# Kernel optimization log

Hardware: AMD Instinct MI355X
Metric: run time of the kernel (lower is better)

## Reference

```python
import jax, jax.numpy as jnp
import numpy as np

NUM_QUERIES = 10000
NUM_CLASSES = 2048
IOU_THRESH = 0.5


def setup_inputs() -> dict:
    key = jax.random.key(0)
    k1, k2, k3, k4 = jax.random.split(key, 4)
    return {
        "pred_logits": jax.random.normal(k1, (1, NUM_QUERIES, NUM_CLASSES), dtype=jnp.float32),
        "pred_boxes": jax.random.uniform(k2, (1, NUM_QUERIES, 4), dtype=jnp.float32),
        "cls_logits": jax.random.normal(k3, (1, NUM_CLASSES), dtype=jnp.float32),
        "target_sizes": jax.random.randint(k4, (1, 2), 480, 1333, dtype=jnp.int64),
    }


def box_cxcywh_to_xyxy(b):
    cx, cy, w, h = b[..., 0], b[..., 1], b[..., 2], b[..., 3]
    return jnp.stack([cx - 0.5 * w, cy - 0.5 * h, cx + 0.5 * w, cy + 0.5 * h], axis=-1)


def nms_keep(boxes, scores, iou_thresh):
    """Greedy NMS; returns a boolean keep mask over the N boxes (xyxy)."""
    n = boxes.shape[0]
    order = jnp.argsort(-scores)
    bs = boxes[order]  # [N,4] sorted by score desc
    areas = jnp.clip(bs[:, 2] - bs[:, 0], 0.0) * jnp.clip(bs[:, 3] - bs[:, 1], 0.0)
    idx = jnp.arange(n)

    def body(i, state):
        keep_s, active = state
        alive = active[i]
        keep_s = keep_s.at[i].set(alive)
        # IoU of box i against all boxes
        lt = jnp.maximum(bs[i, :2], bs[:, :2])
        rb = jnp.minimum(bs[i, 2:], bs[:, 2:])
        wh = jnp.clip(rb - lt, 0.0)
        inter = wh[:, 0] * wh[:, 1]
        iou = inter / (areas[i] + areas - inter)
        suppress = (iou > iou_thresh) & (idx > i) & alive
        return keep_s, active & (~suppress)

    keep_s, _ = jax.lax.fori_loop(
        0, n, body, (jnp.zeros(n, dtype=bool), jnp.ones(n, dtype=bool))
    )
    # map back from sorted order to original order
    return jnp.zeros(n, dtype=bool).at[order].set(keep_s)


def reference(pred_logits, pred_boxes, cls_logits, target_sizes):
    # class scores / labels
    prob = jax.nn.softmax(pred_logits, axis=-1)          # [B,Q,C]
    scores = prob.max(axis=-1)                           # [B,Q]
    labels = prob.argmax(axis=-1)                        # [B,Q]
    cls_preds = jnp.argmax(cls_logits, axis=1)           # [B]

    # boxes: cxcywh -> xyxy, clamp to [0,1], scale to image size
    boxes = jnp.clip(box_cxcywh_to_xyxy(pred_boxes), 0.0, 1.0)  # [B,Q,4]
    ts = target_sizes.astype(jnp.float32)
    img_h, img_w = ts[:, 0], ts[:, 1]
    scale_fct = jnp.stack([img_w, img_h, img_w, img_h], axis=1)  # [B,4]
    boxes = boxes * scale_fct[:, None, :]

    # greedy NMS on batch 0 (module only supports this path for B=1)
    keep = nms_keep(boxes[0], scores.reshape(-1), IOU_THRESH)    # [Q] bool

    return scores[0], labels[0], boxes[0], keep, cls_preds
```

## Files before the change

kernel.cpp:

```cpp
#include <hip/hip_runtime.h>
#include <stdint.h>

#define NQ 10000
#define NC 2048
#define NW 157
#define NR 79
#define IOU_TH 0.5f


__global__ __launch_bounds__(256) void k_scores(const float* __restrict__ logits,
        float* __restrict__ out_scores, float* __restrict__ out_labels,
        float* __restrict__ ws_scores) {
    int wave = threadIdx.x >> 6;
    int lane = threadIdx.x & 63;
    int q = blockIdx.x * 4 + wave;
    if (q >= NQ) return;
    const float* row = logits + (size_t)q * NC;
    float4 v[8];
    float m = -3.4e38f;
    int am = 0;
    #pragma unroll
    for (int k = 0; k < 8; k++) {
        int idx = k * 256 + lane * 4;
        v[k] = *(const float4*)(row + idx);
        if (v[k].x > m) { m = v[k].x; am = idx; }
        if (v[k].y > m) { m = v[k].y; am = idx + 1; }
        if (v[k].z > m) { m = v[k].z; am = idx + 2; }
        if (v[k].w > m) { m = v[k].w; am = idx + 3; }
    }
    #pragma unroll
    for (int off = 32; off >= 1; off >>= 1) {
        float om = __shfl_xor(m, off);
        int   oa = __shfl_xor(am, off);
        if (om > m || (om == m && oa < am)) { m = om; am = oa; }
    }
    float s = 0.f;
    #pragma unroll
    for (int k = 0; k < 8; k++) {
        s += expf(v[k].x - m);
        s += expf(v[k].y - m);
        s += expf(v[k].z - m);
        s += expf(v[k].w - m);
    }
    #pragma unroll
    for (int off = 32; off >= 1; off >>= 1) s += __shfl_xor(s, off);
    if (lane == 0) {
        float sc = 1.0f / s;
        out_scores[q] = sc;
        out_labels[q] = (float)am;
        ws_scores[q]  = sc;
    }
}

__global__ __launch_bounds__(256) void k_cls(const float* __restrict__ cls,
                                             float* __restrict__ out) {
    float m = -3.4e38f; int am = 0x7fffffff;
    for (int idx = threadIdx.x; idx < NC; idx += 256) {
        float x = cls[idx];
        if (x > m) { m = x; am = idx; }
    }
    int lane = threadIdx.x & 63, wave = threadIdx.x >> 6;
    #pragma unroll
    for (int off = 32; off >= 1; off >>= 1) {
        float om = __shfl_xor(m, off); int oa = __shfl_xor(am, off);
        if (om > m || (om == m && oa < am)) { m = om; am = oa; }
    }
    __shared__ float sm[4]; __shared__ int sa[4];
    if (lane == 0) { sm[wave] = m; sa[wave] = am; }
    __syncthreads();
    if (threadIdx.x == 0) {
        for (int w = 1; w < 4; w++)
            if (sm[w] > m || (sm[w] == m && sa[w] < am)) { m = sm[w]; am = sa[w]; }
        out[0] = (float)am;
    }
}

__global__ __launch_bounds__(256) void k_boxes(const float* __restrict__ pb,
        const int* __restrict__ ts, float* __restrict__ out_boxes,
        float* __restrict__ boxes4, int* __restrict__ rank) {
    #pragma clang fp contract(off)
    int i = blockIdx.x * 256 + threadIdx.x;
    if (i >= NQ) return;
    rank[i] = 0;
    int a0 = ts[0], a1 = ts[1];
    int ih, iw;
    if (a1 == 0) { ih = a0; iw = ts[2]; } else { ih = a0; iw = a1; }
    float sh = (float)ih, sw = (float)iw;
    float4 b = *(const float4*)(pb + i * 4);
    float x1 = b.x - 0.5f * b.z;
    float y1 = b.y - 0.5f * b.w;
    float x2 = b.x + 0.5f * b.z;
    float y2 = b.y + 0.5f * b.w;
    x1 = fminf(fmaxf(x1, 0.f), 1.f) * sw;
    y1 = fminf(fmaxf(y1, 0.f), 1.f) * sh;
    x2 = fminf(fmaxf(x2, 0.f), 1.f) * sw;
    y2 = fminf(fmaxf(y2, 0.f), 1.f) * sh;
    float4 o = make_float4(x1, y1, x2, y2);
    *(float4*)(out_boxes + i * 4) = o;
    *(float4*)(boxes4 + i * 4) = o;
}

__global__ __launch_bounds__(256) void k_count(const float* __restrict__ scores,
                                               int* __restrict__ rank) {
    __shared__ float sc[2000];
    int jbase = blockIdx.y * 2000;
    int jn = min(2000, NQ - jbase);
    for (int t = threadIdx.x; t < jn; t += 256) sc[t] = scores[jbase + t];
    __syncthreads();
    int i = blockIdx.x * 256 + threadIdx.x;
    if (i >= NQ) return;
    float si = scores[i];
    int cnt = 0;
    for (int jj = 0; jj < jn; jj++) {
        float sj = sc[jj];
        int j = jbase + jj;
        cnt += (sj > si) || (sj == si && j < i);
    }
    if (cnt) atomicAdd(&rank[i], cnt);
}

__global__ __launch_bounds__(256) void k_scatter(const float* __restrict__ boxes4,
        const int* __restrict__ rank, int* __restrict__ order,
        float* __restrict__ sx1, float* __restrict__ sy1,
        float* __restrict__ sx2, float* __restrict__ sy2,
        float* __restrict__ sarea) {
    #pragma clang fp contract(off)
    int i = blockIdx.x * 256 + threadIdx.x;
    if (i >= NQ) return;
    int r = rank[i];
    order[r] = i;
    float4 b = *(const float4*)(boxes4 + i * 4);
    sx1[r] = b.x; sy1[r] = b.y; sx2[r] = b.z; sy2[r] = b.w;
    sarea[r] = fmaxf(b.z - b.x, 0.f) * fmaxf(b.w - b.y, 0.f);
}

__global__ __launch_bounds__(64) void k_mask(const float* __restrict__ sx1,
        const float* __restrict__ sy1, const float* __restrict__ sx2,
        const float* __restrict__ sy2, const float* __restrict__ sarea,
        unsigned long long* __restrict__ mask) {
    #pragma clang fp contract(off)
    int rb = blockIdx.x, cb = blockIdx.y;
    if (cb < rb) return;
    int t = threadIdx.x;
    __shared__ float cx1[64], cy1[64], cx2[64], cy2[64], ca[64];
    int j0 = cb * 64 + t;
    if (j0 < NQ) { cx1[t]=sx1[j0]; cy1[t]=sy1[j0]; cx2[t]=sx2[j0]; cy2[t]=sy2[j0]; ca[t]=sarea[j0]; }
    __syncthreads();
    int i = rb * 64 + t;
    if (i >= NQ) return;
    float xi1 = sx1[i], yi1 = sy1[i], xi2 = sx2[i], yi2 = sy2[i], ai = sarea[i];
    int ncol = min(64, NQ - cb * 64);
    unsigned long long word = 0;
    for (int jj = 0; jj < ncol; jj++) {
        int j = cb * 64 + jj;
        float lx = fmaxf(xi1, cx1[jj]);
        float ly = fmaxf(yi1, cy1[jj]);
        float rx = fminf(xi2, cx2[jj]);
        float ry = fminf(yi2, cy2[jj]);
        float w = fmaxf(rx - lx, 0.f);
        float h = fmaxf(ry - ly, 0.f);
        float inter = w * h;
        float denom = (ai + ca[jj]) - inter;
        float iou = inter / denom;
        bool sup = (iou > IOU_TH) && (j > i);
        word |= ((unsigned long long)(sup ? 1u : 0u)) << jj;
    }
    mask[(size_t)i * NW + cb] = word;
}

__device__ __forceinline__ unsigned long long bcast64(unsigned long long v) {
    uint32_t lo = (uint32_t)__builtin_amdgcn_readfirstlane((int)(uint32_t)v);
    uint32_t hi = (uint32_t)__builtin_amdgcn_readfirstlane((int)(uint32_t)(v >> 32));
    return ((unsigned long long)hi << 32) | lo;
}

__global__ __launch_bounds__(256, 1) void k_scan(const unsigned long long* __restrict__ mask,
        const int* __restrict__ order, float* __restrict__ out_keep) {
    __shared__ unsigned long long rem[NW];
    __shared__ unsigned long long keepw[NW];
    __shared__ unsigned long long stA[2][4][64];
    __shared__ unsigned long long stB[2][3][64];
    __shared__ unsigned long long sh_k0, sh_k1;

    const int tid  = threadIdx.x;
    const int wave = tid >> 6;
    const int lane = tid & 63;

    for (int w = tid; w < NW; w += 256) rem[w] = 0;

    if (wave == 1) {
        uint64_t sA0=0,sA1=0,sA2=0,sA3=0,sB0=0,sB1=0,sB2=0;
        int ra = lane, rb = 64 + lane;
        {
            const unsigned long long* rp = mask + (size_t)ra * NW;
            sA0 = rp[0]; sA1 = rp[1]; sA2 = rp[2]; sA3 = rp[3];
        }
        {
            const unsigned long long* rp = mask + (size_t)rb * NW;
            sB0 = rp[1]; sB1 = rp[2]; sB2 = rp[3];
        }
        stA[0][0][lane]=sA0; stA[0][1][lane]=sA1; stA[0][2][lane]=sA2; stA[0][3][lane]=sA3;
        stB[0][0][lane]=sB0; stB[0][1][lane]=sB1; stB[0][2][lane]=sB2;
    }
    __syncthreads();

    uint64_t pp0=0,pp1=0,pp2=0,pp3=0,pp4=0,pp5=0,pp6=0,pp7=0;
    uint64_t pp8=0,pp9=0,pp10=0,pp11=0,pp12=0,pp13=0,pp14=0,pp15=0;
    uint64_t pp16=0,pp17=0,pp18=0,pp19=0,pp20=0,pp21=0,pp22=0,pp23=0;
    uint64_t pp24=0,pp25=0,pp26=0,pp27=0,pp28=0,pp29=0,pp30=0,pp31=0;
    uint64_t pex = 0;
    int pw = -1;

    uint64_t kept0 = 0, kept1 = 0;

    for (int r = 0; r < NR; r++) {
        const int a = 2 * r, b = a + 1;
        const int par = r & 1;

        uint64_t sA0=0,sA1=0,sA2=0,sA3=0,sB0=0,sB1=0,sB2=0;

        if (wave == 0) {
            uint64_t remA_v = rem[a];
            uint64_t remB_v = (b < NW) ? rem[b] : ~0ull;
            uint64_t dgA = stA[par][0][lane];
            uint64_t xAB = stA[par][1][lane];
            uint64_t dgB = (b < NW) ? stB[par][0][lane] : 0;

            uint64_t cur0 = bcast64(remA_v);
            int nv0 = min(64, NQ - a * 64);
            if (nv0 < 64) cur0 |= (~0ull) << nv0;
            uint32_t dglo = (uint32_t)dgA, dghi = (uint32_t)(dgA >> 32);
            uint32_t xlo  = (uint32_t)xAB, xhi  = (uint32_t)(xAB >> 32);
            uint64_t alive = ~cur0;
            uint64_t k0 = 0, AcB = 0;
            while (alive) {
                int bb = (int)__builtin_ctzll(alive);
                uint64_t d = ((uint64_t)(uint32_t)__builtin_amdgcn_readlane((int)dghi, bb) << 32)
                           | (uint32_t)__builtin_amdgcn_readlane((int)dglo, bb);
                uint64_t x = ((uint64_t)(uint32_t)__builtin_amdgcn_readlane((int)xhi, bb) << 32)
                           | (uint32_t)__builtin_amdgcn_readlane((int)xlo, bb);
                k0    |= 1ull << bb;
                cur0  |= d;
                AcB   |= x;
                alive &= ~(d | (1ull << bb));
            }
            kept0 = k0;

            uint64_t k1 = 0, cur1 = 0;
            if (b < NW) {
                cur1 = bcast64(remB_v) | AcB;
                int nv1 = min(64, NQ - b * 64);
                if (nv1 < 64) cur1 |= (~0ull) << nv1;
                uint32_t blo = (uint32_t)dgB, bhi = (uint32_t)(dgB >> 32);
                uint64_t alv = ~cur1;
                while (alv) {
                    int bb = (int)__builtin_ctzll(alv);
                    uint64_t d = ((uint64_t)(uint32_t)__builtin_amdgcn_readlane((int)bhi, bb) << 32)
                               | (uint32_t)__builtin_amdgcn_readlane((int)blo, bb);
                    k1  |= 1ull << bb;
                    cur1 |= d;
                    alv &= ~(d | (1ull << bb));
                }
            }
            kept1 = k1;
            if (tid == 0) {
                sh_k0 = k0; sh_k1 = k1;
                keepw[a] = cur0;
                if (b < NW) keepw[b] = cur1;
            }
        } else {
            if (pw >= 0) {
                uint64_t pacc = (((pp0|pp1)|(pp2|pp3)) | ((pp4|pp5)|(pp6|pp7)))
                              | (((pp8|pp9)|(pp10|pp11)) | ((pp12|pp13)|(pp14|pp15)));
                pacc |= (((pp16|pp17)|(pp18|pp19)) | ((pp20|pp21)|(pp22|pp23)))
                      | (((pp24|pp25)|(pp26|pp27)) | ((pp28|pp29)|(pp30|pp31)));
                pacc |= pex;
                if (pacc) atomicOr(&rem[pw], (unsigned long long)pacc);
            }
            pw = -1;

            if (wave == 1) {
                int a2 = a + 2, b2 = a + 3;
                int ra = a2 * 64 + lane, rb = b2 * 64 + lane;
                if (a2 < NW && ra < NQ) {
                    const unsigned long long* rp = mask + (size_t)ra * NW + a2;
                    sA0 = rp[0];
                    if (a2 + 1 < NW) sA1 = rp[1];
                    if (a2 + 2 < NW) sA2 = rp[2];
                    if (a2 + 3 < NW) sA3 = rp[3];
                }
                if (b2 < NW && rb < NQ) {
                    const unsigned long long* rp = mask + (size_t)rb * NW + b2;
                    sB0 = rp[0];
                    if (b2 + 1 < NW) sB1 = rp[1];
                    if (b2 + 2 < NW) sB2 = rp[2];
                }
            }
        }
        __syncthreads();

        const int c2 = a + 2, c3 = a + 3;
        if (wave == 0) {
            if (c2 < NW) {
                uint64_t vA2 = stA[par][2][lane];
                uint64_t vB1 = (b < NW) ? stB[par][1][lane] : 0;
                uint64_t m2 = (((kept0 >> lane) & 1ull) ? vA2 : 0)
                            | (((kept1 >> lane) & 1ull) ? vB1 : 0);
                uint64_t m3 = 0;
                if (c3 < NW) {
                    uint64_t vA3 = stA[par][3][lane];
                    uint64_t vB2 = (b < NW) ? stB[par][2][lane] : 0;
                    m3 = (((kept0 >> lane) & 1ull) ? vA3 : 0)
                       | (((kept1 >> lane) & 1ull) ? vB2 : 0);
                }
                #pragma unroll
                for (int off = 32; off >= 1; off >>= 1) {
                    m2 |= __shfl_xor(m2, off);
                    m3 |= __shfl_xor(m3, off);
                }
                if (lane == 0) {
                    rem[c2] |= m2;
                    if (c3 < NW) rem[c3] |= m3;
                }
            }
        } else {
            uint64_t k0 = bcast64(sh_k0);
            uint64_t k1 = bcast64(sh_k1);

            if (wave == 1) {
                int par2 = (r + 1) & 1;
                stA[par2][0][lane]=sA0; stA[par2][1][lane]=sA1;
                stA[par2][2][lane]=sA2; stA[par2][3][lane]=sA3;
                stB[par2][0][lane]=sB0; stB[par2][1][lane]=sB1; stB[par2][2][lane]=sB2;
            }

            int w = a + 4 + (tid - 64);
            if ((k0 | k1) && w < NW) {
                const unsigned long long* baseA = mask + (size_t)(a * 64) * NW + w;
                const unsigned long long* baseB = mask + (size_t)(b * 64) * NW + w;
                uint64_t km0 = k0, km1 = k1;
                const unsigned long long* fb =
                    km0 ? baseA + (size_t)__builtin_ctzll(km0) * NW
                        : baseB + (size_t)__builtin_ctzll(km1) * NW;
                #define BULK_SLOT(P) { const unsigned long long* rp; \
                    if (km0)      { rp = baseA + (size_t)__builtin_ctzll(km0) * NW; km0 &= km0 - 1; } \
                    else if (km1) { rp = baseB + (size_t)__builtin_ctzll(km1) * NW; km1 &= km1 - 1; } \
                    else rp = fb; \
                    P = rp[0]; }
                BULK_SLOT(pp0)  BULK_SLOT(pp1)  BULK_SLOT(pp2)  BULK_SLOT(pp3)
                BULK_SLOT(pp4)  BULK_SLOT(pp5)  BULK_SLOT(pp6)  BULK_SLOT(pp7)
                BULK_SLOT(pp8)  BULK_SLOT(pp9)  BULK_SLOT(pp10) BULK_SLOT(pp11)
                BULK_SLOT(pp12) BULK_SLOT(pp13) BULK_SLOT(pp14) BULK_SLOT(pp15)
                BULK_SLOT(pp16) BULK_SLOT(pp17) BULK_SLOT(pp18) BULK_SLOT(pp19)
                BULK_SLOT(pp20) BULK_SLOT(pp21) BULK_SLOT(pp22) BULK_SLOT(pp23)
                BULK_SLOT(pp24) BULK_SLOT(pp25) BULK_SLOT(pp26) BULK_SLOT(pp27)
                BULK_SLOT(pp28) BULK_SLOT(pp29) BULK_SLOT(pp30) BULK_SLOT(pp31)
                pex = 0;
                while (km0 | km1) {
                    uint64_t x0,x1,x2,x3,x4,x5,x6,x7;
                    BULK_SLOT(x0) BULK_SLOT(x1) BULK_SLOT(x2) BULK_SLOT(x3)
                    BULK_SLOT(x4) BULK_SLOT(x5) BULK_SLOT(x6) BULK_SLOT(x7)
                    pex |= (x0|x1)|(x2|x3)|((x4|x5)|(x6|x7));
                }
                #undef BULK_SLOT
                pw = w;
            } else {
                pw = -1; pex = 0;
            }
        }
        __syncthreads();
    }

    for (int si = tid; si < NQ; si += 256) {
        unsigned long long kw = keepw[si >> 6];
        out_keep[order[si]] = ((kw >> (si & 63)) & 1ull) ? 0.f : 1.f;
    }
}

extern "C" void kernel_launch(void* const* d_in, const int* in_sizes, int n_in,
                              void* d_out, int out_size, void* d_ws, size_t ws_size,
                              hipStream_t stream) {
    const float* pred_logits = (const float*)d_in[0];
    const float* pred_boxes  = (const float*)d_in[1];
    const float* cls_logits  = (const float*)d_in[2];
    const int*   tsizes      = (const int*)d_in[3];

    float* out = (float*)d_out;
    float* out_scores = out;
    float* out_labels = out + 10000;
    float* out_boxes  = out + 20000;
    float* out_keep   = out + 60000;
    float* out_cls    = out + 70000;

    char* ws = (char*)d_ws;
    float* ws_scores = (float*)(ws + 0);
    int*   rank      = (int*)  (ws + 40000);
    float* boxes4    = (float*)(ws + 80000);
    float* sx1       = (float*)(ws + 240000);
    float* sy1       = (float*)(ws + 280000);
    float* sx2       = (float*)(ws + 320000);
    float* sy2       = (float*)(ws + 360000);
    float* sarea     = (float*)(ws + 400000);
    int*   order     = (int*)  (ws + 440000);
    unsigned long long* mask = (unsigned long long*)(ws + 480000);

    k_scores<<<2500, 256, 0, stream>>>(pred_logits, out_scores, out_labels, ws_scores);
    k_cls<<<1, 256, 0, stream>>>(cls_logits, out_cls);
    k_boxes<<<40, 256, 0, stream>>>(pred_boxes, tsizes, out_boxes, boxes4, rank);
    k_count<<<dim3(40, 5), 256, 0, stream>>>(ws_scores, rank);
    k_scatter<<<40, 256, 0, stream>>>(boxes4, rank, order, sx1, sy1, sx2, sy2, sarea);
    k_mask<<<dim3(157, 157), 64, 0, stream>>>(sx1, sy1, sx2, sy2, sarea, mask);
    k_scan<<<1, 256, 0, stream>>>(mask, order, out_keep);
}
```

Baseline: 440.6 us.

## Fuse front kernels, triangular mask grid, vectorize rank count, deepen scan prefetch

Merges the score, class-argmax and box kernels into one launch so fewer small kernels run back to back. The IoU mask kernel now launches only upper-triangle blocks, with the row and column block recovered from the linear index via a sqrt, instead of launching the full square grid and exiting half the blocks. The rank-count loop reads scores as float4 from shared memory. The scan kernel prefetches mask rows two rounds ahead from the bulk waves and folds the self bit into the diagonal word to shorten the greedy inner loop. This adds branching inside the fused kernel and a double-precision sqrt per mask block.

```diff
diff --git a/kernel.cpp b/kernel.cpp
--- a/kernel.cpp
+++ b/kernel.cpp
@@ -1,120 +1,130 @@
 #include <hip/hip_runtime.h>
 #include <stdint.h>
+#include <math.h>
 
 #define NQ 10000
 #define NC 2048
 #define NW 157
 #define NR 79
+#define NTRI 12403
 #define IOU_TH 0.5f
 
 
-__global__ __launch_bounds__(256) void k_scores(const float* __restrict__ logits,
+__global__ __launch_bounds__(256) void k_front(const float* __restrict__ logits,
+        const float* __restrict__ cls, const float* __restrict__ pb,
+        const int* __restrict__ ts,
         float* __restrict__ out_scores, float* __restrict__ out_labels,
-        float* __restrict__ ws_scores) {
-    int wave = threadIdx.x >> 6;
-    int lane = threadIdx.x & 63;
-    int q = blockIdx.x * 4 + wave;
-    if (q >= NQ) return;
-    const float* row = logits + (size_t)q * NC;
-    float4 v[8];
-    float m = -3.4e38f;
-    int am = 0;
-    #pragma unroll
-    for (int k = 0; k < 8; k++) {
-        int idx = k * 256 + lane * 4;
-        v[k] = *(const float4*)(row + idx);
-        if (v[k].x > m) { m = v[k].x; am = idx; }
-        if (v[k].y > m) { m = v[k].y; am = idx + 1; }
-        if (v[k].z > m) { m = v[k].z; am = idx + 2; }
-        if (v[k].w > m) { m = v[k].w; am = idx + 3; }
-    }
-    #pragma unroll
-    for (int off = 32; off >= 1; off >>= 1) {
-        float om = __shfl_xor(m, off);
-        int   oa = __shfl_xor(am, off);
-        if (om > m || (om == m && oa < am)) { m = om; am = oa; }
-    }
-    float s = 0.f;
-    #pragma unroll
-    for (int k = 0; k < 8; k++) {
-        s += expf(v[k].x - m);
-        s += expf(v[k].y - m);
-        s += expf(v[k].z - m);
-        s += expf(v[k].w - m);
-    }
-    #pragma unroll
-    for (int off = 32; off >= 1; off >>= 1) s += __shfl_xor(s, off);
-    if (lane == 0) {
-        float sc = 1.0f / s;
-        out_scores[q] = sc;
-        out_labels[q] = (float)am;
-        ws_scores[q]  = sc;
-    }
-}
-
-__global__ __launch_bounds__(256) void k_cls(const float* __restrict__ cls,
-                                             float* __restrict__ out) {
-    float m = -3.4e38f; int am = 0x7fffffff;
-    for (int idx = threadIdx.x; idx < NC; idx += 256) {
-        float x = cls[idx];
-        if (x > m) { m = x; am = idx; }
-    }
-    int lane = threadIdx.x & 63, wave = threadIdx.x >> 6;
-    #pragma unroll
-    for (int off = 32; off >= 1; off >>= 1) {
-        float om = __shfl_xor(m, off); int oa = __shfl_xor(am, off);
-        if (om > m || (om == m && oa < am)) { m = om; am = oa; }
-    }
-    __shared__ float sm[4]; __shared__ int sa[4];
-    if (lane == 0) { sm[wave] = m; sa[wave] = am; }
-    __syncthreads();
-    if (threadIdx.x == 0) {
-        for (int w = 1; w < 4; w++)
-            if (sm[w] > m || (sm[w] == m && sa[w] < am)) { m = sm[w]; am = sa[w]; }
-        out[0] = (float)am;
-    }
-}
-
-__global__ __launch_bounds__(256) void k_boxes(const float* __restrict__ pb,
-        const int* __restrict__ ts, float* __restrict__ out_boxes,
-        float* __restrict__ boxes4, int* __restrict__ rank) {
-    #pragma clang fp contract(off)
-    int i = blockIdx.x * 256 + threadIdx.x;
-    if (i >= NQ) return;
-    rank[i] = 0;
-    int a0 = ts[0], a1 = ts[1];
-    int ih, iw;
-    if (a1 == 0) { ih = a0; iw = ts[2]; } else { ih = a0; iw = a1; }
-    float sh = (float)ih, sw = (float)iw;
-    float4 b = *(const float4*)(pb + i * 4);
-    float x1 = b.x - 0.5f * b.z;
-    float y1 = b.y - 0.5f * b.w;
-    float x2 = b.x + 0.5f * b.z;
-    float y2 = b.y + 0.5f * b.w;
-    x1 = fminf(fmaxf(x1, 0.f), 1.f) * sw;
-    y1 = fminf(fmaxf(y1, 0.f), 1.f) * sh;
-    x2 = fminf(fmaxf(x2, 0.f), 1.f) * sw;
-    y2 = fminf(fmaxf(y2, 0.f), 1.f) * sh;
-    float4 o = make_float4(x1, y1, x2, y2);
-    *(float4*)(out_boxes + i * 4) = o;
-    *(float4*)(boxes4 + i * 4) = o;
+        float* __restrict__ out_cls, float* __restrict__ out_boxes,
+        float* __restrict__ ws_scores, float* __restrict__ boxes4,
+        int* __restrict__ rank) {
+    int bx = blockIdx.x;
+    if (bx < 2500) {
+        int wave = threadIdx.x >> 6;
+        int lane = threadIdx.x & 63;
+        int q = bx * 4 + wave;
+        if (q >= NQ) return;
+        const float* row = logits + (size_t)q * NC;
+        float4 v[8];
+        float m = -3.4e38f;
+        int am = 0;
+        #pragma unroll
+        for (int k = 0; k < 8; k++) {
+            int idx = k * 256 + lane * 4;
+            v[k] = *(const float4*)(row + idx);
+            if (v[k].x > m) { m = v[k].x; am = idx; }
+            if (v[k].y > m) { m = v[k].y; am = idx + 1; }
+            if (v[k].z > m) { m = v[k].z; am = idx + 2; }
+            if (v[k].w > m) { m = v[k].w; am = idx + 3; }
+        }
+        #pragma unroll
+        for (int off = 32; off >= 1; off >>= 1) {
+            float om = __shfl_xor(m, off);
+            int   oa = __shfl_xor(am, off);
+            if (om > m || (om == m && oa < am)) { m = om; am = oa; }
+        }
+        float s = 0.f;
+        #pragma unroll
+        for (int k = 0; k < 8; k++) {
+            s += expf(v[k].x - m);
+            s += expf(v[k].y - m);
+            s += expf(v[k].z - m);
+            s += expf(v[k].w - m);
+        }
+        #pragma unroll
+        for (int off = 32; off >= 1; off >>= 1) s += __shfl_xor(s, off);
+        if (lane == 0) {
+            float sc = 1.0f / s;
+            out_scores[q] = sc;
+            out_labels[q] = (float)am;
+            ws_scores[q]  = sc;
+        }
+        return;
+    }
+    if (bx == 2500) {
+        float m = -3.4e38f; int am = 0x7fffffff;
+        for (int idx = threadIdx.x; idx < NC; idx += 256) {
+            float x = cls[idx];
+            if (x > m) { m = x; am = idx; }
+        }
+        int lane = threadIdx.x & 63, wave = threadIdx.x >> 6;
+        #pragma unroll
+        for (int off = 32; off >= 1; off >>= 1) {
+            float om = __shfl_xor(m, off); int oa = __shfl_xor(am, off);
+            if (om > m || (om == m && oa < am)) { m = om; am = oa; }
+        }
+        __shared__ float sm[4]; __shared__ int sa[4];
+        if (lane == 0) { sm[wave] = m; sa[wave] = am; }
+        __syncthreads();
+        if (threadIdx.x == 0) {
+            for (int w = 1; w < 4; w++)
+                if (sm[w] > m || (sm[w] == m && sa[w] < am)) { m = sm[w]; am = sa[w]; }
+            out_cls[0] = (float)am;
+        }
+        return;
+    }
+    {
+        #pragma clang fp contract(off)
+        int i = (bx - 2501) * 256 + threadIdx.x;
+        if (i >= NQ) return;
+        rank[i] = 0;
+        int a0 = ts[0], a1 = ts[1];
+        int ih, iw;
+        if (a1 == 0) { ih = a0; iw = ts[2]; } else { ih = a0; iw = a1; }
+        float sh = (float)ih, sw = (float)iw;
+        float4 b = *(const float4*)(pb + i * 4);
+        float x1 = b.x - 0.5f * b.z;
+        float y1 = b.y - 0.5f * b.w;
+        float x2 = b.x + 0.5f * b.z;
+        float y2 = b.y + 0.5f * b.w;
+        x1 = fminf(fmaxf(x1, 0.f), 1.f) * sw;
+        y1 = fminf(fmaxf(y1, 0.f), 1.f) * sh;
+        x2 = fminf(fmaxf(x2, 0.f), 1.f) * sw;
+        y2 = fminf(fmaxf(y2, 0.f), 1.f) * sh;
+        float4 o = make_float4(x1, y1, x2, y2);
+        *(float4*)(out_boxes + i * 4) = o;
+        *(float4*)(boxes4 + i * 4) = o;
+    }
 }
 
 __global__ __launch_bounds__(256) void k_count(const float* __restrict__ scores,
                                                int* __restrict__ rank) {
-    __shared__ float sc[2000];
+    __shared__ float4 sc4[500];
     int jbase = blockIdx.y * 2000;
-    int jn = min(2000, NQ - jbase);
-    for (int t = threadIdx.x; t < jn; t += 256) sc[t] = scores[jbase + t];
+    const float4* src = (const float4*)(scores + jbase);
+    for (int t = threadIdx.x; t < 500; t += 256) sc4[t] = src[t];
     __syncthreads();
     int i = blockIdx.x * 256 + threadIdx.x;
     if (i >= NQ) return;
     float si = scores[i];
     int cnt = 0;
-    for (int jj = 0; jj < jn; jj++) {
-        float sj = sc[jj];
-        int j = jbase + jj;
-        cnt += (sj > si) || (sj == si && j < i);
+    #pragma unroll 2
+    for (int q = 0; q < 500; q++) {
+        float4 v = sc4[q];
+        int j = jbase + 4 * q;
+        cnt += (v.x > si) || (v.x == si && j     < i);
+        cnt += (v.y > si) || (v.y == si && j + 1 < i);
+        cnt += (v.z > si) || (v.z == si && j + 2 < i);
+        cnt += (v.w > si) || (v.w == si && j + 3 < i);
     }
     if (cnt) atomicAdd(&rank[i], cnt);
 }
@@ -139,8 +149,13 @@
         const float* __restrict__ sy2, const float* __restrict__ sarea,
         unsigned long long* __restrict__ mask) {
     #pragma clang fp contract(off)
-    int rb = blockIdx.x, cb = blockIdx.y;
-    if (cb < rb) return;
+    int tri = blockIdx.x;
+    int rb = (int)((2.0 * NW + 1.0
+              - sqrt((double)((2 * NW + 1) * (2 * NW + 1) - 8 * tri))) * 0.5);
+    while (rb > 0 && rb * NW - rb * (rb - 1) / 2 > tri) rb--;
+    while ((rb + 1) * NW - (rb + 1) * rb / 2 <= tri) rb++;
+    int cb = rb + (tri - (rb * NW - rb * (rb - 1) / 2));
+
     int t = threadIdx.x;
     __shared__ float cx1[64], cy1[64], cx2[64], cy2[64], ca[64];
     int j0 = cb * 64 + t;
@@ -188,19 +203,22 @@
 
     for (int w = tid; w < NW; w += 256) rem[w] = 0;
 
+    uint64_t sA0=0,sA1=0,sA2=0,sA3=0,sB0=0,sB1=0,sB2=0;
+
     if (wave == 1) {
-        uint64_t sA0=0,sA1=0,sA2=0,sA3=0,sB0=0,sB1=0,sB2=0;
-        int ra = lane, rb = 64 + lane;
         {
-            const unsigned long long* rp = mask + (size_t)ra * NW;
-            sA0 = rp[0]; sA1 = rp[1]; sA2 = rp[2]; sA3 = rp[3];
+            const unsigned long long* rp = mask + (size_t)lane * NW;
+            stA[0][0][lane]=rp[0]; stA[0][1][lane]=rp[1];
+            stA[0][2][lane]=rp[2]; stA[0][3][lane]=rp[3];
+            const unsigned long long* rq = mask + (size_t)(64 + lane) * NW;
+            stB[0][0][lane]=rq[1]; stB[0][1][lane]=rq[2]; stB[0][2][lane]=rq[3];
         }
         {
-            const unsigned long long* rp = mask + (size_t)rb * NW;
-            sB0 = rp[1]; sB1 = rp[2]; sB2 = rp[3];
-        }
-        stA[0][0][lane]=sA0; stA[0][1][lane]=sA1; stA[0][2][lane]=sA2; stA[0][3][lane]=sA3;
-        stB[0][0][lane]=sB0; stB[0][1][lane]=sB1; stB[0][2][lane]=sB2;
+            const unsigned long long* rp = mask + (size_t)(128 + lane) * NW + 2;
+            sA0=rp[0]; sA1=rp[1]; sA2=rp[2]; sA3=rp[3];
+            const unsigned long long* rq = mask + (size_t)(192 + lane) * NW + 3;
+            sB0=rq[0]; sB1=rq[1]; sB2=rq[2];
+        }
     }
     __syncthreads();
 
@@ -217,33 +235,34 @@
         const int a = 2 * r, b = a + 1;
         const int par = r & 1;
 
-        uint64_t sA0=0,sA1=0,sA2=0,sA3=0,sB0=0,sB1=0,sB2=0;
-
         if (wave == 0) {
             uint64_t remA_v = rem[a];
             uint64_t remB_v = (b < NW) ? rem[b] : ~0ull;
             uint64_t dgA = stA[par][0][lane];
             uint64_t xAB = stA[par][1][lane];
             uint64_t dgB = (b < NW) ? stB[par][0][lane] : 0;
+            uint64_t dfA = dgA | (1ull << lane);
+            uint64_t dfB = dgB | (1ull << lane);
 
             uint64_t cur0 = bcast64(remA_v);
             int nv0 = min(64, NQ - a * 64);
             if (nv0 < 64) cur0 |= (~0ull) << nv0;
-            uint32_t dglo = (uint32_t)dgA, dghi = (uint32_t)(dgA >> 32);
+            uint32_t dflo = (uint32_t)dfA, dfhi = (uint32_t)(dfA >> 32);
             uint32_t xlo  = (uint32_t)xAB, xhi  = (uint32_t)(xAB >> 32);
             uint64_t alive = ~cur0;
             uint64_t k0 = 0, AcB = 0;
             while (alive) {
                 int bb = (int)__builtin_ctzll(alive);
-                uint64_t d = ((uint64_t)(uint32_t)__builtin_amdgcn_readlane((int)dghi, bb) << 32)
-                           | (uint32_t)__builtin_amdgcn_readlane((int)dglo, bb);
-                uint64_t x = ((uint64_t)(uint32_t)__builtin_amdgcn_readlane((int)xhi, bb) << 32)
-                           | (uint32_t)__builtin_amdgcn_readlane((int)xlo, bb);
+                uint64_t df = ((uint64_t)(uint32_t)__builtin_amdgcn_readlane((int)dfhi, bb) << 32)
+                            | (uint32_t)__builtin_amdgcn_readlane((int)dflo, bb);
+                uint64_t x  = ((uint64_t)(uint32_t)__builtin_amdgcn_readlane((int)xhi, bb) << 32)
+                            | (uint32_t)__builtin_amdgcn_readlane((int)xlo, bb);
                 k0    |= 1ull << bb;
-                cur0  |= d;
+                cur0  |= df;
                 AcB   |= x;
-                alive &= ~(d | (1ull << bb));
-            }
+                alive &= ~df;
+            }
+            cur0 &= ~k0;
             kept0 = k0;
 
             uint64_t k1 = 0, cur1 = 0;
@@ -251,16 +270,17 @@
                 cur1 = bcast64(remB_v) | AcB;
                 int nv1 = min(64, NQ - b * 64);
                 if (nv1 < 64) cur1 |= (~0ull) << nv1;
-                uint32_t blo = (uint32_t)dgB, bhi = (uint32_t)(dgB >> 32);
+                uint32_t blo = (uint32_t)dfB, bhi = (uint32_t)(dfB >> 32);
                 uint64_t alv = ~cur1;
                 while (alv) {
                     int bb = (int)__builtin_ctzll(alv);
-                    uint64_t d = ((uint64_t)(uint32_t)__builtin_amdgcn_readlane((int)bhi, bb) << 32)
-                               | (uint32_t)__builtin_amdgcn_readlane((int)blo, bb);
+                    uint64_t df = ((uint64_t)(uint32_t)__builtin_amdgcn_readlane((int)bhi, bb) << 32)
+                                | (uint32_t)__builtin_amdgcn_readlane((int)blo, bb);
                     k1  |= 1ull << bb;
-                    cur1 |= d;
-                    alv &= ~(d | (1ull << bb));
-                }
+                    cur1 |= df;
+                    alv &= ~df;
+                }
+                cur1 &= ~k1;
             }
             kept1 = k1;
             if (tid == 0) {
@@ -278,24 +298,6 @@
                 if (pacc) atomicOr(&rem[pw], (unsigned long long)pacc);
             }
             pw = -1;
-
-            if (wave == 1) {
-                int a2 = a + 2, b2 = a + 3;
-                int ra = a2 * 64 + lane, rb = b2 * 64 + lane;
-                if (a2 < NW && ra < NQ) {
-                    const unsigned long long* rp = mask + (size_t)ra * NW + a2;
-                    sA0 = rp[0];
-                    if (a2 + 1 < NW) sA1 = rp[1];
-                    if (a2 + 2 < NW) sA2 = rp[2];
-                    if (a2 + 3 < NW) sA3 = rp[3];
-                }
-                if (b2 < NW && rb < NQ) {
-                    const unsigned long long* rp = mask + (size_t)rb * NW + b2;
-                    sB0 = rp[0];
-                    if (b2 + 1 < NW) sB1 = rp[1];
-                    if (b2 + 2 < NW) sB2 = rp[2];
-                }
-            }
         }
         __syncthreads();
 
@@ -332,6 +334,25 @@
                 stA[par2][0][lane]=sA0; stA[par2][1][lane]=sA1;
                 stA[par2][2][lane]=sA2; stA[par2][3][lane]=sA3;
                 stB[par2][0][lane]=sB0; stB[par2][1][lane]=sB1; stB[par2][2][lane]=sB2;
+                sA0=sA1=sA2=sA3=sB0=sB1=sB2=0;
+                int rr = r + 2;
+                if (rr < NR) {
+                    int a2 = 2 * rr, b2 = a2 + 1;
+                    int ra = a2 * 64 + lane, rbw = b2 * 64 + lane;
+                    if (a2 < NW && ra < NQ) {
+                        const unsigned long long* rp = mask + (size_t)ra * NW + a2;
+                        sA0 = rp[0];
+                        if (a2 + 1 < NW) sA1 = rp[1];
+                        if (a2 + 2 < NW) sA2 = rp[2];
+                        if (a2 + 3 < NW) sA3 = rp[3];
+                    }
+                    if (b2 < NW && rbw < NQ) {
+                        const unsigned long long* rq = mask + (size_t)rbw * NW + b2;
+                        sB0 = rq[0];
+                        if (b2 + 1 < NW) sB1 = rq[1];
+                        if (b2 + 2 < NW) sB2 = rq[2];
+                    }
+                }
             }
 
             int w = a + 4 + (tid - 64);
@@ -404,11 +425,11 @@
     int*   order     = (int*)  (ws + 440000);
     unsigned long long* mask = (unsigned long long*)(ws + 480000);
 
-    k_scores<<<2500, 256, 0, stream>>>(pred_logits, out_scores, out_labels, ws_scores);
-    k_cls<<<1, 256, 0, stream>>>(cls_logits, out_cls);
-    k_boxes<<<40, 256, 0, stream>>>(pred_boxes, tsizes, out_boxes, boxes4, rank);
+    k_front<<<2541, 256, 0, stream>>>(pred_logits, cls_logits, pred_boxes, tsizes,
+                                      out_scores, out_labels, out_cls, out_boxes,
+                                      ws_scores, boxes4, rank);
     k_count<<<dim3(40, 5), 256, 0, stream>>>(ws_scores, rank);
     k_scatter<<<40, 256, 0, stream>>>(boxes4, rank, order, sx1, sy1, sx2, sy2, sarea);
-    k_mask<<<dim3(157, 157), 64, 0, stream>>>(sx1, sy1, sx2, sy2, sarea, mask);
+    k_mask<<<NTRI, 64, 0, stream>>>(sx1, sy1, sx2, sy2, sarea, mask);
     k_scan<<<1, 256, 0, stream>>>(mask, order, out_keep);
 }
```

After: 423.8 us. 1.04x faster.
